# Optimization experiments

Measured on AMD Instinct MI355X. Metric: run time of the kernel, lower is better.

Reference implementation:

```python
import jax, jax.numpy as jnp
import numpy as np

IN_C, OUT_C, K, STRIDE, PAD = 64, 128, 3, 1, 1


def setup_inputs() -> dict:
    key = jax.random.key(0)
    kx, kw = jax.random.split(key)
    x = jax.random.normal(kx, (16, IN_C, 112, 112), dtype=jnp.float32)
    scale = np.sqrt(2.0 / (IN_C * K * K)).astype(np.float32)
    weight = jax.random.normal(kw, (OUT_C, IN_C, K, K), dtype=jnp.float32) * scale
    bias = jnp.zeros((OUT_C,), dtype=jnp.float32)
    return {"x": x, "weight": weight, "bias": bias}


def reference(x, weight, bias):
    # Direct 2D convolution (cross-correlation, like torch Conv2d), NCHW layout.
    out = jax.lax.conv_general_dilated(
        x, weight,
        window_strides=(STRIDE, STRIDE),
        padding=((PAD, PAD), (PAD, PAD)),
        dimension_numbers=("NCHW", "OIHW", "NCHW"),
    )
    return out + bias[None, :, None, None]
```

## Files before the change

### kernel.cpp

```cpp
#include <hip/hip_runtime.h>
#include <stdint.h>


#define HW     112
#define PIX    12544
#define ICN    64
#define OCN    128
#define KDIM   576
#define TILEP  128
#define PTILES 98
#define NBLK   1568
#define LDS_LD 40

typedef __attribute__((ext_vector_type(8))) __bf16 bf16x8;
typedef __attribute__((ext_vector_type(4))) float  f32x4;

__device__ __forceinline__ uint32_t rne_bf16(uint32_t u) {
    return (u + 0x7fffu + ((u >> 16) & 1u)) >> 16;
}

__global__ void prep_weights(const float* __restrict__ w, uint16_t* __restrict__ wt) {
    int idx = blockIdx.x * 256 + threadIdx.x;
    int oc  = idx / KDIM;
    int rem = idx - oc * KDIM;
    int r   = rem >> 6;
    int ic  = rem & 63;
    uint32_t u = __builtin_bit_cast(uint32_t, w[oc * KDIM + ic * 9 + r]);
    wt[idx] = (uint16_t)rne_bf16(u);
}

__global__ void __launch_bounds__(256)
conv_mfma(const float* __restrict__ x, const uint16_t* __restrict__ wt,
          const float* __restrict__ bias, float* __restrict__ out) {
    __shared__ uint16_t As[OCN * LDS_LD];
    __shared__ uint16_t Xs[TILEP * LDS_LD];

    const int t = threadIdx.x;
    const int b = blockIdx.x;
    const int n_img = b / PTILES;
    const int p0 = (b - n_img * PTILES) * TILEP;

    const int sm    = t & 127;
    const int shalf = t >> 7;
    const int sp = p0 + sm;
    const int sh = sp / HW;
    const int sw = sp - sh * HW;
    const float* xn = x + (size_t)n_img * (ICN * PIX);

    const int woc = t >> 1;
    const int wch = (t & 1) * 2;

    const int lane = t & 63;
    const int wave = t >> 6;
    const int lr = lane & 15;
    const int lq = lane >> 4;
    const int oc_base = (wave & 1) * 64;
    const int px_base = (wave >> 1) * 64;

    f32x4 acc[4][4];
    {
        f32x4 z = {0.f, 0.f, 0.f, 0.f};
#pragma unroll
        for (int i = 0; i < 4; ++i)
#pragma unroll
            for (int j = 0; j < 4; ++j) acc[i][j] = z;
    }

    for (int kb = 0; kb < 18; ++kb) {
        const int r  = kb >> 1;
        const int dy = (r / 3) - 1;
        const int dx = (r - (r / 3) * 3) - 1;

        uint4 wv0, wv1;
        {
            const uint4* gsrc = (const uint4*)(wt + (size_t)woc * KDIM + kb * 32);
            wv0 = gsrc[wch];
            wv1 = gsrc[wch + 1];
        }
        const int hh = sh + dy;
        const int ww = sw + dx;
        const bool valid = ((unsigned)hh < HW) & ((unsigned)ww < HW);
        const float* xsrc = xn + (size_t)((kb & 1) * 32 + shalf * 16) * PIX + hh * HW + ww;
        uint32_t pk[8];
#pragma unroll
        for (int j = 0; j < 8; ++j) {
            float f0 = valid ? xsrc[(2 * j) * PIX] : 0.0f;
            float f1 = valid ? xsrc[(2 * j + 1) * PIX] : 0.0f;
            uint32_t u0 = rne_bf16(__builtin_bit_cast(uint32_t, f0));
            uint32_t u1 = __builtin_bit_cast(uint32_t, f1);
            u1 = (u1 + 0x7fffu + ((u1 >> 16) & 1u)) & 0xffff0000u;
            pk[j] = u0 | u1;
        }

        __syncthreads();
        {
            char* wdst = (char*)As + woc * (LDS_LD * 2);
            *(uint4*)(wdst + wch * 16)       = wv0;
            *(uint4*)(wdst + (wch + 1) * 16) = wv1;
        }
        {
            char* xdst = (char*)Xs + sm * (LDS_LD * 2) + shalf * 32;
            *(uint4*)(xdst)      = make_uint4(pk[0], pk[1], pk[2], pk[3]);
            *(uint4*)(xdst + 16) = make_uint4(pk[4], pk[5], pk[6], pk[7]);
        }
        __syncthreads();

        bf16x8 a_frag[4], b_frag[4];
#pragma unroll
        for (int mi = 0; mi < 4; ++mi)
            a_frag[mi] = *(const bf16x8*)((const char*)As +
                          (oc_base + mi * 16 + lr) * (LDS_LD * 2) + lq * 16);
#pragma unroll
        for (int ni = 0; ni < 4; ++ni)
            b_frag[ni] = *(const bf16x8*)((const char*)Xs +
                          (px_base + ni * 16 + lr) * (LDS_LD * 2) + lq * 16);

#pragma unroll
        for (int mi = 0; mi < 4; ++mi)
#pragma unroll
            for (int ni = 0; ni < 4; ++ni)
                acc[mi][ni] = __builtin_amdgcn_mfma_f32_16x16x32_bf16(
                    a_frag[mi], b_frag[ni], acc[mi][ni], 0, 0, 0);
    }

#pragma unroll
    for (int mi = 0; mi < 4; ++mi) {
#pragma unroll
        for (int rg = 0; rg < 4; ++rg) {
            const int oc = oc_base + mi * 16 + lq * 4 + rg;
            const float bb = bias[oc];
            float* orow = out + ((size_t)n_img * OCN + oc) * PIX + p0 + px_base + lr;
#pragma unroll
            for (int ni = 0; ni < 4; ++ni)
                orow[ni * 16] = acc[mi][ni][rg] + bb;
        }
    }
}

extern "C" void kernel_launch(void* const* d_in, const int* in_sizes, int n_in,
                              void* d_out, int out_size, void* d_ws, size_t ws_size,
                              hipStream_t stream) {
    const float* x    = (const float*)d_in[0];
    const float* w    = (const float*)d_in[1];
    const float* bias = (const float*)d_in[2];
    float* out = (float*)d_out;
    uint16_t* wt = (uint16_t*)d_ws;

    prep_weights<<<288, 256, 0, stream>>>(w, wt);
    conv_mfma<<<NBLK, 256, 0, stream>>>(x, wt, bias, out);
}
```

Baseline: 210.5 us.

## Pre-transpose input to NHWC bf16 and stage tiles via direct global-to-LDS loads

A prep kernel now converts the whole input once into a pixel-major bf16 layout (64 channels, 128 bytes per pixel) and lays the weights out per tap. The conv kernel then stages each tap's 64-channel slice with global_load_lds 16-byte loads into XOR-swizzled LDS. Padding is handled by pointing out-of-bounds loads at a zeroed buffer. This removes the strided fp32 NCHW gathers and the per-tap bf16 conversion from the main loop, and halves the number of barrier pairs. The cost is an extra pass that writes and rereads about 25 MB of transposed input, plus a larger LDS footprint.

```diff
diff --git a/kernel.cpp b/kernel.cpp
--- a/kernel.cpp
+++ b/kernel.cpp
@@ -6,49 +6,88 @@
 #define PIX    12544
 #define ICN    64
 #define OCN    128
-#define KDIM   576
 #define TILEP  128
 #define PTILES 98
 #define NBLK   1568
-#define LDS_LD 40
+#define NIMG   16
+
+#define XT_BYTES   (NIMG * PIX * ICN * 2)
+#define WT_OFF     XT_BYTES
+#define WT_BYTES   (9 * OCN * ICN * 2)
+#define ZG_OFF     (WT_OFF + WT_BYTES)
+#define XBLK       (NIMG * (PIX / 64))
+#define WBLK       72
 
 typedef __attribute__((ext_vector_type(8))) __bf16 bf16x8;
 typedef __attribute__((ext_vector_type(4))) float  f32x4;
 
-__device__ __forceinline__ uint32_t rne_bf16(uint32_t u) {
+__device__ __forceinline__ uint32_t rne_lo(float f) {
+    uint32_t u = __builtin_bit_cast(uint32_t, f);
     return (u + 0x7fffu + ((u >> 16) & 1u)) >> 16;
 }
+__device__ __forceinline__ uint32_t pk2(float a, float b) {
+    uint32_t ub = __builtin_bit_cast(uint32_t, b);
+    ub = (ub + 0x7fffu + ((ub >> 16) & 1u)) & 0xffff0000u;
+    return rne_lo(a) | ub;
+}
 
-__global__ void prep_weights(const float* __restrict__ w, uint16_t* __restrict__ wt) {
-    int idx = blockIdx.x * 256 + threadIdx.x;
-    int oc  = idx / KDIM;
-    int rem = idx - oc * KDIM;
-    int r   = rem >> 6;
-    int ic  = rem & 63;
-    uint32_t u = __builtin_bit_cast(uint32_t, w[oc * KDIM + ic * 9 + r]);
-    wt[idx] = (uint16_t)rne_bf16(u);
+__device__ __forceinline__ void load_lds16(const void* g, void* l) {
+    __builtin_amdgcn_global_load_lds(
+        (const __attribute__((address_space(1))) uint32_t*)g,
+        (__attribute__((address_space(3))) uint32_t*)l, 16, 0, 0);
 }
 
 __global__ void __launch_bounds__(256)
-conv_mfma(const float* __restrict__ x, const uint16_t* __restrict__ wt,
-          const float* __restrict__ bias, float* __restrict__ out) {
-    __shared__ uint16_t As[OCN * LDS_LD];
-    __shared__ uint16_t Xs[TILEP * LDS_LD];
+prep(const float* __restrict__ x, const float* __restrict__ w, uint8_t* __restrict__ ws) {
+    const int b = blockIdx.x;
+    const int t = threadIdx.x;
+    uint16_t* xt = (uint16_t*)ws;
+    uint16_t* wt = (uint16_t*)(ws + WT_OFF);
+
+    if (b < XBLK) {
+        const int n  = b / (PIX / 64);
+        const int p0 = (b - n * (PIX / 64)) * 64;
+        const int px = t >> 2;
+        const int q  = t & 3;
+        const float* src = x + ((size_t)n * ICN + q * 16) * PIX + p0 + px;
+        float v[16];
+#pragma unroll
+        for (int i = 0; i < 16; ++i) v[i] = src[(size_t)i * PIX];
+        uint4 u0 = make_uint4(pk2(v[0], v[1]),  pk2(v[2], v[3]),
+                              pk2(v[4], v[5]),  pk2(v[6], v[7]));
+        uint4 u1 = make_uint4(pk2(v[8], v[9]),  pk2(v[10], v[11]),
+                              pk2(v[12], v[13]), pk2(v[14], v[15]));
+        char* dst = (char*)xt + ((size_t)(n * PIX + p0 + px)) * 128 + q * 32;
+        *(uint4*)dst        = u0;
+        *(uint4*)(dst + 16) = u1;
+    } else {
+        const int wb = b - XBLK;
+#pragma unroll
+        for (int k = 0; k < 4; ++k) {
+            int wi = wb * 1024 + k * 256 + t;
+            int r  = wi >> 13;
+            int oc = (wi >> 6) & 127;
+            int ic = wi & 63;
+            wt[wi] = (uint16_t)rne_lo(w[oc * 576 + ic * 9 + r]);
+        }
+        if (wb == 0 && t < 8) ((uint4*)(ws + ZG_OFF))[t] = make_uint4(0, 0, 0, 0);
+    }
+}
+
+__global__ void __launch_bounds__(256)
+conv_mfma(const uint8_t* __restrict__ ws, const float* __restrict__ bias,
+          float* __restrict__ out) {
+    __shared__ uint16_t As[8192];
+    __shared__ uint16_t Xs[8192];
+
+    const char* xt = (const char*)ws;
+    const char* wt = (const char*)(ws + WT_OFF);
+    const char* zg = (const char*)(ws + ZG_OFF);
 
     const int t = threadIdx.x;
     const int b = blockIdx.x;
     const int n_img = b / PTILES;
     const int p0 = (b - n_img * PTILES) * TILEP;
-
-    const int sm    = t & 127;
-    const int shalf = t >> 7;
-    const int sp = p0 + sm;
-    const int sh = sp / HW;
-    const int sw = sp - sh * HW;
-    const float* xn = x + (size_t)n_img * (ICN * PIX);
-
-    const int woc = t >> 1;
-    const int wch = (t & 1) * 2;
 
     const int lane = t & 63;
     const int wave = t >> 6;
@@ -56,6 +95,22 @@
     const int lq = lane >> 4;
     const int oc_base = (wave & 1) * 64;
     const int px_base = (wave >> 1) * 64;
+
+    const int rowB = t >> 3;
+    const int cswz = (t & 7) ^ (rowB & 7);
+    int sh[4], sw[4];
+    const char* xaddr[4];
+#pragma unroll
+    for (int r2 = 0; r2 < 4; ++r2) {
+        int row = r2 * 32 + rowB;
+        int p = p0 + row;
+        int hh = p / HW;
+        sh[r2] = hh;
+        sw[r2] = p - hh * HW;
+        xaddr[r2] = xt + ((size_t)(n_img * PIX + p)) * 128 + cswz * 16;
+    }
+    const char* waddr0 = wt + rowB * 128 + cswz * 16;
+    const char* zaddr  = zg + (t & 7) * 16;
 
     f32x4 acc[4][4];
     {
@@ -66,61 +121,50 @@
             for (int j = 0; j < 4; ++j) acc[i][j] = z;
     }
 
-    for (int kb = 0; kb < 18; ++kb) {
-        const int r  = kb >> 1;
-        const int dy = (r / 3) - 1;
-        const int dx = (r - (r / 3) * 3) - 1;
+#pragma unroll
+    for (int tap = 0; tap < 9; ++tap) {
+        const int dy = tap / 3 - 1;
+        const int dx = tap - (tap / 3) * 3 - 1;
+        const int toff = (dy * HW + dx) * 128;
 
-        uint4 wv0, wv1;
-        {
-            const uint4* gsrc = (const uint4*)(wt + (size_t)woc * KDIM + kb * 32);
-            wv0 = gsrc[wch];
-            wv1 = gsrc[wch + 1];
-        }
-        const int hh = sh + dy;
-        const int ww = sw + dx;
-        const bool valid = ((unsigned)hh < HW) & ((unsigned)ww < HW);
-        const float* xsrc = xn + (size_t)((kb & 1) * 32 + shalf * 16) * PIX + hh * HW + ww;
-        uint32_t pk[8];
+        __syncthreads();
+
 #pragma unroll
-        for (int j = 0; j < 8; ++j) {
-            float f0 = valid ? xsrc[(2 * j) * PIX] : 0.0f;
-            float f1 = valid ? xsrc[(2 * j + 1) * PIX] : 0.0f;
-            uint32_t u0 = rne_bf16(__builtin_bit_cast(uint32_t, f0));
-            uint32_t u1 = __builtin_bit_cast(uint32_t, f1);
-            u1 = (u1 + 0x7fffu + ((u1 >> 16) & 1u)) & 0xffff0000u;
-            pk[j] = u0 | u1;
+        for (int r2 = 0; r2 < 4; ++r2)
+            load_lds16(waddr0 + tap * 16384 + r2 * 4096,
+                       (char*)As + r2 * 4096 + wave * 1024);
+#pragma unroll
+        for (int r2 = 0; r2 < 4; ++r2) {
+            int hh = sh[r2] + dy;
+            int wwp = sw[r2] + dx;
+            bool ok = ((unsigned)hh < HW) & ((unsigned)wwp < HW);
+            const char* gp = ok ? (xaddr[r2] + toff) : zaddr;
+            load_lds16(gp, (char*)Xs + r2 * 4096 + wave * 1024);
         }
 
         __syncthreads();
-        {
-            char* wdst = (char*)As + woc * (LDS_LD * 2);
-            *(uint4*)(wdst + wch * 16)       = wv0;
-            *(uint4*)(wdst + (wch + 1) * 16) = wv1;
-        }
-        {
-            char* xdst = (char*)Xs + sm * (LDS_LD * 2) + shalf * 32;
-            *(uint4*)(xdst)      = make_uint4(pk[0], pk[1], pk[2], pk[3]);
-            *(uint4*)(xdst + 16) = make_uint4(pk[4], pk[5], pk[6], pk[7]);
-        }
-        __syncthreads();
-
-        bf16x8 a_frag[4], b_frag[4];
-#pragma unroll
-        for (int mi = 0; mi < 4; ++mi)
-            a_frag[mi] = *(const bf16x8*)((const char*)As +
-                          (oc_base + mi * 16 + lr) * (LDS_LD * 2) + lq * 16);
-#pragma unroll
-        for (int ni = 0; ni < 4; ++ni)
-            b_frag[ni] = *(const bf16x8*)((const char*)Xs +
-                          (px_base + ni * 16 + lr) * (LDS_LD * 2) + lq * 16);
 
 #pragma unroll
-        for (int mi = 0; mi < 4; ++mi)
+        for (int kh = 0; kh < 2; ++kh) {
+            bf16x8 a_frag[4], b_frag[4];
+            const int cc = kh * 4 + lq;
 #pragma unroll
-            for (int ni = 0; ni < 4; ++ni)
-                acc[mi][ni] = __builtin_amdgcn_mfma_f32_16x16x32_bf16(
-                    a_frag[mi], b_frag[ni], acc[mi][ni], 0, 0, 0);
+            for (int mi = 0; mi < 4; ++mi) {
+                int R = oc_base + mi * 16 + lr;
+                a_frag[mi] = *(const bf16x8*)((const char*)As + R * 128 + ((cc ^ (R & 7)) * 16));
+            }
+#pragma unroll
+            for (int ni = 0; ni < 4; ++ni) {
+                int R = px_base + ni * 16 + lr;
+                b_frag[ni] = *(const bf16x8*)((const char*)Xs + R * 128 + ((cc ^ (R & 7)) * 16));
+            }
+#pragma unroll
+            for (int mi = 0; mi < 4; ++mi)
+#pragma unroll
+                for (int ni = 0; ni < 4; ++ni)
+                    acc[mi][ni] = __builtin_amdgcn_mfma_f32_16x16x32_bf16(
+                        a_frag[mi], b_frag[ni], acc[mi][ni], 0, 0, 0);
+        }
     }
 
 #pragma unroll
@@ -144,8 +188,8 @@
     const float* w    = (const float*)d_in[1];
     const float* bias = (const float*)d_in[2];
     float* out = (float*)d_out;
-    uint16_t* wt = (uint16_t*)d_ws;
+    uint8_t* ws = (uint8_t*)d_ws;
 
-    prep_weights<<<288, 256, 0, stream>>>(w, wt);
-    conv_mfma<<<NBLK, 256, 0, stream>>>(x, wt, bias, out);
+    prep<<<XBLK + WBLK, 256, 0, stream>>>(x, w, ws);
+    conv_mfma<<<NBLK, 256, 0, stream>>>(ws, bias, out);
 }
```

Measured after the change: 174.4 us. -17.2%, faster.
